# Kernel tuning notes

Hardware: AMD Instinct MI355X
Metric: run time of the kernel (lower is better)

The kernel has to match this reference:

```python
import jax, jax.numpy as jnp
import numpy as np
from jax import lax

NJ = 14
COL = 14
SIGMA = 1.0
RADIUS = 4  # scipy gaussian_filter: truncate=4.0 * sigma=1.0 -> radius 4


def _gauss_kernel():
    x = np.arange(-RADIUS, RADIUS + 1, dtype=np.float32)
    w = np.exp(-0.5 * x * x / (SIGMA * SIGMA))
    w /= w.sum()
    return jnp.asarray(w)


def _blur(delta):
    # separable gaussian with scipy mode='reflect' (== np.pad 'symmetric')
    B, J, H, W = delta.shape
    w = _gauss_kernel()
    p = jnp.pad(delta, ((0, 0), (0, 0), (RADIUS, RADIUS), (RADIUS, RADIUS)), mode='symmetric')
    lhs = p.reshape(B * J, 1, H + 2 * RADIUS, W + 2 * RADIUS)
    kh = w.reshape(1, 1, 2 * RADIUS + 1, 1)
    kw = w.reshape(1, 1, 1, 2 * RADIUS + 1)
    dn = ('NCHW', 'OIHW', 'NCHW')
    y = lax.conv_general_dilated(lhs, kh, (1, 1), 'VALID', dimension_numbers=dn)
    y = lax.conv_general_dilated(y, kw, (1, 1), 'VALID', dimension_numbers=dn)
    return y.reshape(B, J, H, W)


def setup_inputs() -> dict:
    key = jax.random.key(0)
    k1, k2, k3, k4 = jax.random.split(key, 4)
    B = 8192
    o = jax.random.normal(k1, (B, 2 * NJ, COL, COL), jnp.float32)
    h = jax.random.uniform(k2, (B, NJ, COL, COL), jnp.float32)
    t = jax.random.uniform(k3, (B, NJ, 2), jnp.float32)
    vis = jax.random.randint(k4, (B, NJ), 0, 2).astype(jnp.float32)
    v = jnp.repeat(vis[..., None], 2, axis=-1)  # visibility duplicated over (x,y)
    return {"o": o, "h": h, "t": t, "v": v}


def reference(o, h, t, v):
    B = h.shape[0]
    scale = 1.0 / float(COL)
    f32 = jnp.float32

    # argmax coordinate extraction from predicted heatmaps
    argmax = jnp.argmax(h.reshape(B, NJ, COL * COL), axis=-1)  # [B,Nj]
    yC = argmax // COL
    xC = argmax - yC * COL
    bidx = jnp.arange(B)[:, None]
    jidx = jnp.arange(NJ)[None, :]

    h_peak = h[bidx, jidx, yC, xC]                 # [B,Nj]
    cond = h_peak > 0.5
    ox = o[bidx, jidx, yC, xC]                     # offset channels 0..Nj-1
    oy = o[bidx, jidx + NJ, yC, xC]                # offset channels Nj..2Nj-1
    x0 = jnp.where(cond, (ox + xC.astype(f32)) * scale, 0.0)
    x1 = jnp.where(cond, (oy + yC.astype(f32)) * scale, 0.0)
    x = jnp.stack([x0, x1], axis=-1)               # [B,Nj,2]

    # per-joint gaussian target heatmap (only where visible)
    ti = t * COL
    xi = jnp.clip(ti[..., 0].astype(jnp.int32), 0, COL - 1)
    yi = jnp.clip(ti[..., 1].astype(jnp.int32), 0, COL - 1)
    visf = (v[..., 0].astype(jnp.int32) == 1).astype(f32)  # [B,Nj]
    delta = jnp.zeros((B, NJ, COL, COL), f32).at[bidx, jidx, yi, xi].set(visf)
    g = _blur(delta)
    mn = g.min(axis=(-2, -1), keepdims=True)
    mx = g.max(axis=(-2, -1), keepdims=True)
    denom = jnp.where(mx > mn, mx - mn, 1.0)
    tt = jnp.where(visf[..., None, None] > 0, (g - mn) / denom, 0.0)

    # heatmap loss; original zeroes only ROW 0 of diff for invisible joints
    diff1 = h - tt
    row0 = diff1[:, :, 0:1, :] * visf[:, :, None, None]
    diff1 = jnp.concatenate([row0, diff1[:, :, 1:, :]], axis=2)
    N1 = v.sum() / 2.0
    d1 = jnp.sum(diff1 * diff1) / N1

    # coordinate loss
    diff2 = (x - t) * v
    d2 = jnp.sum(diff2 * diff2) / N1  # N2 == N1 in the original
    return d1 + d2
```

## Files before the change

### kernel.cpp

```cpp
#include <hip/hip_runtime.h>

#define NJ    14
#define TILE  196
#define BLK   256
#define JPB   64
#define STAGE_DW (JPB * TILE)

typedef __attribute__((address_space(1))) const void g_void;
typedef __attribute__((address_space(3))) void lds_void;

__device__ __forceinline__ float gtap(int d) {
  const int d2 = d * d;
  const float e = exp2f(-0.72134752044448169f * (float)d2);
  return (d2 <= 16) ? e : 0.0f;
}

__device__ __forceinline__ float uresp(int p, int pk) {
  float s = gtap(p - pk);
  if (p <= 3)  s += gtap(p + pk + 1);
  if (p >= 10) s += gtap(27 - p - pk);
  return s;
}

__device__ __forceinline__ float wave_sum(float x) {
#pragma unroll
  for (int off = 32; off >= 1; off >>= 1) x += __shfl_xor(x, off);
  return x;
}

template<int K>
__device__ __forceinline__ void accum_part(const float4* __restrict__ hp,
    const float (&uy)[14], const float (&ux)[14],
    float& bm, int& bi, float& sh2, float& cross, float& q0)
{
  float rd[14] = {0,0,0,0,0,0,0,0,0,0,0,0,0,0};
  const int NI = (K == 0) ? 13 : 12;
#pragma unroll
  for (int i = 0; i < NI; ++i) {
    const int f = 4 * i + K;
    const float4 q = hp[f];
    const float qa[4] = {q.x, q.y, q.z, q.w};
#pragma unroll
    for (int c = 0; c < 4; ++c) {
      const int idx = 4 * f + c;
      const int y = idx / 14;
      const int x = idx - 14 * y;
      const float hv = qa[c];
      if (hv > bm) { bm = hv; bi = idx; }
      sh2 = fmaf(hv, hv, sh2);
      if (y == 0) q0 = fmaf(hv, hv, q0);
      rd[y] = fmaf(hv, ux[x], rd[y]);
    }
  }
#pragma unroll
  for (int y = 0; y < 14; ++y) cross = fmaf(uy[y], rd[y], cross);
}

__global__ __launch_bounds__(BLK, 3) void joint_kernel(
    const float* __restrict__ o, const float* __restrict__ h,
    const float* __restrict__ t, const float* __restrict__ v,
    float2* __restrict__ part)
{
  __shared__ __align__(16) float lds[STAGE_DW];
  __shared__ float rs[4], rn[4];

  const int tid  = threadIdx.x;
  const int lane = tid & 63;
  const int wid  = tid >> 6;
  const int jg   = blockIdx.x * JPB + lane;

  const float* gbase = h + (size_t)blockIdx.x * JPB * TILE;
#pragma unroll
  for (int i = 0; i < 13; ++i) {
    const int idx = i * BLK + tid;
    if (idx < JPB * 49) {
      __builtin_amdgcn_global_load_lds(
          (g_void*)(gbase + (size_t)idx * 4),
          (lds_void*)&lds[idx * 4],
          16, 0, 0);
    }
  }

  float uy[14], ux[14];
  const float2 tv = ((const float2*)t)[jg];
  const int xi = min(max((int)(tv.x * 14.0f), 0), 13);
  const int yi = min(max((int)(tv.y * 14.0f), 0), 13);
#pragma unroll
  for (int p = 0; p < 14; ++p) { uy[p] = uresp(p, yi); ux[p] = uresp(p, xi); }

  asm volatile("s_waitcnt vmcnt(0)" ::: "memory");
  __syncthreads();

  float bm = -3.0e38f; int bi = 0;
  float sh2 = 0.0f, cross = 0.0f, q0 = 0.0f;
  {
    const float4* hp = (const float4*)&lds[lane * TILE];
    switch (wid) {
      case 0: accum_part<0>(hp, uy, ux, bm, bi, sh2, cross, q0); break;
      case 1: accum_part<1>(hp, uy, ux, bm, bi, sh2, cross, q0); break;
      case 2: accum_part<2>(hp, uy, ux, bm, bi, sh2, cross, q0); break;
      default: accum_part<3>(hp, uy, ux, bm, bi, sh2, cross, q0); break;
    }
  }

  __syncthreads();
  float* red = lds;
  red[0 * BLK + tid] = bm;
  ((int*)lds)[1 * BLK + tid] = bi;
  red[2 * BLK + tid] = sh2;
  red[3 * BLK + tid] = cross;
  red[4 * BLK + tid] = q0;
  __syncthreads();

  float s_acc = 0.0f, n_acc = 0.0f;
  if ((lane >> 4) == wid) {
    float Bm = red[lane]; int Bi = ((int*)lds)[BLK + lane];
    float S2 = red[2 * BLK + lane], Cr = red[3 * BLK + lane], Q0 = red[4 * BLK + lane];
#pragma unroll
    for (int w = 1; w < 4; ++w) {
      const float m = red[w * 64 + lane];
      const int   i = ((int*)lds)[BLK + w * 64 + lane];
      if (m > Bm || (m == Bm && i < Bi)) { Bm = m; Bi = i; }
      S2 += red[2 * BLK + w * 64 + lane];
      Cr += red[3 * BLK + w * 64 + lane];
      Q0 += red[4 * BLK + w * 64 + lane];
    }

    const float2 vv = ((const float2*)v)[jg];
    const bool vis = ((int)vv.x) == 1;

    float Sy2 = 0.0f, Sx2 = 0.0f;
#pragma unroll
    for (int p = 0; p < 14; ++p) {
      Sy2 = fmaf(uy[p], uy[p], Sy2);
      Sx2 = fmaf(ux[p], ux[p], Sx2);
    }
    const float maxy = 1.0f + gtap(2 * yi + 1) + gtap(27 - 2 * yi);
    const float maxx = 1.0f + gtap(2 * xi + 1) + gtap(27 - 2 * xi);
    const float inv = vis ? (1.0f / (maxy * maxx)) : 0.0f;

    float s = S2 - 2.0f * inv * Cr + inv * inv * Sy2 * Sx2;
    if (!vis) s -= Q0;

    const int b = jg / NJ;
    const int j = jg - b * NJ;
    const int yC = Bi / 14;
    const int xC = Bi - 14 * yC;
    const size_t ob = ((size_t)b * (2 * NJ) + j) * TILE + (size_t)Bi;
    const float ox = o[ob];
    const float oy = o[ob + (size_t)NJ * TILE];
    const bool cond = Bm > 0.5f;
    const float sc = 1.0f / 14.0f;
    const float px = cond ? (ox + (float)xC) * sc : 0.0f;
    const float py = cond ? (oy + (float)yC) * sc : 0.0f;
    const float d0 = (px - tv.x) * vv.x;
    const float d1 = (py - tv.y) * vv.y;
    s += d0 * d0 + d1 * d1;

    s_acc = s;
    n_acc = vv.x + vv.y;
  }

  s_acc = wave_sum(s_acc);
  n_acc = wave_sum(n_acc);
  if (lane == 0) { rs[wid] = s_acc; rn[wid] = n_acc; }
  __syncthreads();
  if (tid == 0) {
    const float S = rs[0] + rs[1] + rs[2] + rs[3];
    const float N = rn[0] + rn[1] + rn[2] + rn[3];
    part[blockIdx.x] = make_float2(S, N);
  }
}

#define FBLK 1024
__global__ __launch_bounds__(FBLK) void finalize_kernel(
    const float2* __restrict__ part, float* __restrict__ out, int nblocks)
{
  float s = 0.0f, n = 0.0f;
  for (int i = threadIdx.x; i < nblocks; i += FBLK) {
    const float2 p = part[i];
    s += p.x;
    n += p.y;
  }
  s = wave_sum(s);
  n = wave_sum(n);
  __shared__ float rs[16], rn[16];
  const int lane = threadIdx.x & 63, wid = threadIdx.x >> 6;
  if (lane == 0) { rs[wid] = s; rn[wid] = n; }
  __syncthreads();
  if (threadIdx.x == 0) {
    float S = 0.0f, N = 0.0f;
#pragma unroll
    for (int i = 0; i < 16; ++i) { S += rs[i]; N += rn[i]; }
    out[0] = S / (0.5f * N);
  }
}

extern "C" void kernel_launch(void* const* d_in, const int* in_sizes, int n_in,
                              void* d_out, int out_size, void* d_ws, size_t ws_size,
                              hipStream_t stream)
{
  const float* o = (const float*)d_in[0];
  const float* h = (const float*)d_in[1];
  const float* t = (const float*)d_in[2];
  const float* v = (const float*)d_in[3];
  const int njoint = in_sizes[1] / TILE;
  const int nblocks = njoint / JPB;

  float2* part = (float2*)d_ws;
  joint_kernel<<<nblocks, BLK, 0, stream>>>(o, h, t, v, part);
  finalize_kernel<<<1, FBLK, 0, stream>>>(part, (float*)d_out, nblocks);
}
```

Before: 28.73 us.

## Shrink blocks to 16 joints over two waves with direct cross accumulation

Each block now handles 16 joints with 2 waves of 128 threads instead of 64 joints with 4 waves, so there are four times as many blocks and each one stages much less LDS. Only 16 lanes of each wave do the per-joint accumulation, and the per-row reduction array is replaced by a direct FMA with uy*ux. The aim is more blocks in flight and lower per-block LDS and register pressure. The cost is that 75% of lanes sit idle during the main compute phase, and there are more partials for the finalize kernel to sum.

```diff
diff --git a/kernel.cpp b/kernel.cpp
--- a/kernel.cpp
+++ b/kernel.cpp
@@ -2,9 +2,9 @@
 
 #define NJ    14
 #define TILE  196
-#define BLK   256
-#define JPB   64
-#define STAGE_DW (JPB * TILE)
+#define BLK   128
+#define JPB   16
+#define N4    (JPB * 49)
 
 typedef __attribute__((address_space(1))) const void g_void;
 typedef __attribute__((address_space(3))) void lds_void;
@@ -28,16 +28,15 @@
   return x;
 }
 
-template<int K>
+template<int P>
 __device__ __forceinline__ void accum_part(const float4* __restrict__ hp,
     const float (&uy)[14], const float (&ux)[14],
     float& bm, int& bi, float& sh2, float& cross, float& q0)
 {
-  float rd[14] = {0,0,0,0,0,0,0,0,0,0,0,0,0,0};
-  const int NI = (K == 0) ? 13 : 12;
+  const int NI = (P == 0) ? 25 : 24;
 #pragma unroll
   for (int i = 0; i < NI; ++i) {
-    const int f = 4 * i + K;
+    const int f = 2 * i + P;
     const float4 q = hp[f];
     const float qa[4] = {q.x, q.y, q.z, q.w};
 #pragma unroll
@@ -49,31 +48,30 @@
       if (hv > bm) { bm = hv; bi = idx; }
       sh2 = fmaf(hv, hv, sh2);
       if (y == 0) q0 = fmaf(hv, hv, q0);
-      rd[y] = fmaf(hv, ux[x], rd[y]);
-    }
-  }
-#pragma unroll
-  for (int y = 0; y < 14; ++y) cross = fmaf(uy[y], rd[y], cross);
-}
-
-__global__ __launch_bounds__(BLK, 3) void joint_kernel(
+      cross = fmaf(hv, uy[y] * ux[x], cross);
+    }
+  }
+}
+
+__global__ __launch_bounds__(BLK, 4) void joint_kernel(
     const float* __restrict__ o, const float* __restrict__ h,
     const float* __restrict__ t, const float* __restrict__ v,
     float2* __restrict__ part)
 {
-  __shared__ __align__(16) float lds[STAGE_DW];
-  __shared__ float rs[4], rn[4];
+  __shared__ __align__(16) float lds[N4 * 4];
+  __shared__ float rs[2], rn[2];
 
   const int tid  = threadIdx.x;
   const int lane = tid & 63;
   const int wid  = tid >> 6;
-  const int jg   = blockIdx.x * JPB + lane;
+  const int jl   = lane & 15;
+  const int jg   = blockIdx.x * JPB + jl;
 
   const float* gbase = h + (size_t)blockIdx.x * JPB * TILE;
 #pragma unroll
-  for (int i = 0; i < 13; ++i) {
+  for (int i = 0; i < 7; ++i) {
     const int idx = i * BLK + tid;
-    if (idx < JPB * 49) {
+    if (idx < N4) {
       __builtin_amdgcn_global_load_lds(
           (g_void*)(gbase + (size_t)idx * 4),
           (lds_void*)&lds[idx * 4],
@@ -93,38 +91,34 @@
 
   float bm = -3.0e38f; int bi = 0;
   float sh2 = 0.0f, cross = 0.0f, q0 = 0.0f;
-  {
-    const float4* hp = (const float4*)&lds[lane * TILE];
-    switch (wid) {
-      case 0: accum_part<0>(hp, uy, ux, bm, bi, sh2, cross, q0); break;
-      case 1: accum_part<1>(hp, uy, ux, bm, bi, sh2, cross, q0); break;
-      case 2: accum_part<2>(hp, uy, ux, bm, bi, sh2, cross, q0); break;
-      default: accum_part<3>(hp, uy, ux, bm, bi, sh2, cross, q0); break;
-    }
+  if (lane < 16) {
+    const float4* hp = (const float4*)&lds[jl * TILE];
+    if (wid == 0) accum_part<0>(hp, uy, ux, bm, bi, sh2, cross, q0);
+    else          accum_part<1>(hp, uy, ux, bm, bi, sh2, cross, q0);
   }
 
   __syncthreads();
   float* red = lds;
-  red[0 * BLK + tid] = bm;
-  ((int*)lds)[1 * BLK + tid] = bi;
-  red[2 * BLK + tid] = sh2;
-  red[3 * BLK + tid] = cross;
-  red[4 * BLK + tid] = q0;
+  if (lane < 16) {
+    red[0 * 32 + wid * 16 + jl] = bm;
+    ((int*)lds)[1 * 32 + wid * 16 + jl] = bi;
+    red[2 * 32 + wid * 16 + jl] = sh2;
+    red[3 * 32 + wid * 16 + jl] = cross;
+    red[4 * 32 + wid * 16 + jl] = q0;
+  }
   __syncthreads();
 
   float s_acc = 0.0f, n_acc = 0.0f;
-  if ((lane >> 4) == wid) {
-    float Bm = red[lane]; int Bi = ((int*)lds)[BLK + lane];
-    float S2 = red[2 * BLK + lane], Cr = red[3 * BLK + lane], Q0 = red[4 * BLK + lane];
-#pragma unroll
-    for (int w = 1; w < 4; ++w) {
-      const float m = red[w * 64 + lane];
-      const int   i = ((int*)lds)[BLK + w * 64 + lane];
+  if (lane < 16 && (lane >> 3) == wid) {
+    float Bm = red[0 * 32 + jl];       int Bi = ((int*)lds)[1 * 32 + jl];
+    {
+      const float m = red[0 * 32 + 16 + jl];
+      const int   i = ((int*)lds)[1 * 32 + 16 + jl];
       if (m > Bm || (m == Bm && i < Bi)) { Bm = m; Bi = i; }
-      S2 += red[2 * BLK + w * 64 + lane];
-      Cr += red[3 * BLK + w * 64 + lane];
-      Q0 += red[4 * BLK + w * 64 + lane];
-    }
+    }
+    const float S2 = red[2 * 32 + jl] + red[2 * 32 + 16 + jl];
+    const float Cr = red[3 * 32 + jl] + red[3 * 32 + 16 + jl];
+    const float Q0 = red[4 * 32 + jl] + red[4 * 32 + 16 + jl];
 
     const float2 vv = ((const float2*)v)[jg];
     const bool vis = ((int)vv.x) == 1;
@@ -165,11 +159,7 @@
   n_acc = wave_sum(n_acc);
   if (lane == 0) { rs[wid] = s_acc; rn[wid] = n_acc; }
   __syncthreads();
-  if (tid == 0) {
-    const float S = rs[0] + rs[1] + rs[2] + rs[3];
-    const float N = rn[0] + rn[1] + rn[2] + rn[3];
-    part[blockIdx.x] = make_float2(S, N);
-  }
+  if (tid == 0) part[blockIdx.x] = make_float2(rs[0] + rs[1], rn[0] + rn[1]);
 }
 
 #define FBLK 1024
```

Result: slower. 46.53 us (+62.0%).
